# Kernel optimization log

Measured on AMD Instinct MI355X. Metric: run time of the kernel, lower is better.

Reference implementation:

```python
import jax, jax.numpy as jnp
import numpy as np

B, S, D, E, H, K = 64, 2048, 1024, 32, 4096, 8


def setup_inputs() -> dict:
    key = jax.random.key(0)
    k0, k1, k2, k3 = jax.random.split(key, 4)
    x = jax.random.normal(k0, (B, S, D), jnp.float32)
    # gate: nn.Linear(D, E) -> weight [E, D], bias [E]
    gate_w = jax.random.normal(k1, (E, D), jnp.float32) * (1.0 / np.sqrt(D))
    gate_b = jnp.zeros((E,), jnp.float32)
    # expert weights include the bias row (input dim + 1)
    w1 = jax.random.normal(k2, (E, D + 1, H), jnp.float32) * (1.0 / np.sqrt(D + 1))
    w2 = jax.random.normal(k3, (E, H + 1, D), jnp.float32) * (1.0 / np.sqrt(H + 1))
    return {"x": x, "gate_w": gate_w, "gate_b": gate_b, "w1": w1, "w2": w2}


def reference(x, gate_w, gate_b, w1, w2):
    b, s, d = x.shape
    # gating: softmax over the TOKEN axis (expert-choice routing)
    logits = jnp.einsum('bsd,ed->bse', x, gate_w) + gate_b          # [b, s, E]
    probs = jax.nn.softmax(logits, axis=-2)                          # softmax over tokens
    # top-k tokens per expert (torch.topk over dim=-2)
    vals_t, idx_t = jax.lax.top_k(probs.transpose(0, 2, 1), K)      # [b, E, k]
    vals = vals_t.transpose(0, 2, 1)                                 # [b, k, E]
    idx = idx_t.transpose(0, 2, 1)                                   # [b, k, E]
    flat_idx = idx.reshape(b, K * E)                                 # gather order: [k, E] flattened
    # gather selected tokens
    tok = jnp.take_along_axis(x, flat_idx[:, :, None], axis=1)       # [b, k*E, d]
    tok = tok.reshape(b, K, E, d)
    # weighted merge (mux) of the k tokens per expert
    merged = jnp.einsum('bked,bke->bed', tok, vals)                  # [b, E, d]
    ones = jnp.ones(merged.shape[:-1] + (1,), merged.dtype)
    # expert FFN (bias folded into the extra weight row)
    h = jnp.einsum('bei,eih->beh', jnp.concatenate([merged, ones], -1), w1)
    h = jax.nn.gelu(h, approximate=False)                            # torch nn.GELU() = exact erf
    o = jnp.einsum('bej,ejo->beo', jnp.concatenate([h, ones], -1), w2)  # [b, E, d]
    # demux: broadcast expert output back to its k tokens, weighted, scatter-add
    out_tok = jnp.einsum('beo,bke->bkeo', o, vals).reshape(b, K * E, d)
    out = jnp.zeros_like(x).at[jnp.arange(b)[:, None], flat_idx].add(out_tok)
    return out
```

## Files before the change

### kernel.cpp

```cpp
#include <hip/hip_runtime.h>
#include <hip/hip_bf16.h>
#include <math.h>

constexpr int NB = 64;
constexpr int NS = 2048;
constexpr int ND = 1024;
constexpr int NE = 32;
constexpr int NH = 4096;
constexpr int NK = 8;

typedef short bf16x8 __attribute__((ext_vector_type(8)));
typedef float f32x4  __attribute__((ext_vector_type(4)));

__device__ __forceinline__ unsigned short f2bf_rne(float v) {
  unsigned u = __builtin_bit_cast(unsigned, v);
  u += 0x7fffu + ((u >> 16) & 1u);
  return (unsigned short)(u >> 16);
}

__device__ __forceinline__ void gload_lds16(const void* g, void* l) {
  __builtin_amdgcn_global_load_lds(
      (const __attribute__((address_space(1))) unsigned*)g,
      (__attribute__((address_space(3))) unsigned*)l, 16, 0, 0);
}

__global__ __launch_bounds__(256) void k_gate_mfma(const float* __restrict__ x,
                                                   const float* __restrict__ gw,
                                                   float* __restrict__ logitsT) {
  const int b  = blockIdx.y;
  const int s0 = blockIdx.x * 128;
  const int t  = threadIdx.x;
  const int l  = t & 63;
  const int w  = t >> 6;

  __shared__ char smem[40960];
  float* trans = (float*)smem;

  f32x4 acc[2][2] = {};

  const int xr_ = t >> 4, xc = (t & 15) * 4;
  const int ge = t >> 3,  gk = (t & 7) * 8;

  float xA[8][4], xB[8][4], wA[8], wB[8];

  auto issue = [&](int kt, float (&xreg)[8][4], float (&wreg)[8]) {
    const int k0 = kt * 64;
#pragma unroll
    for (int p = 0; p < 8; ++p) {
      const int r = p * 16 + xr_;
      *(float4*)xreg[p] = *(const float4*)&x[((size_t)b * NS + s0 + r) * ND + k0 + xc];
    }
    *(float4*)&wreg[0] = *(const float4*)&gw[(size_t)ge * ND + k0 + gk];
    *(float4*)&wreg[4] = *(const float4*)&gw[(size_t)ge * ND + k0 + gk + 4];
  };
  auto commit = [&](int dst, float (&xreg)[8][4], float (&wreg)[8]) {
    short* Ah = (short*)(smem + dst * 16384);
    short* Bh = (short*)(smem + 32768 + dst * 4096);
#pragma unroll
    for (int p = 0; p < 8; ++p) {
      const int r = p * 16 + xr_;
      unsigned short h[4];
#pragma unroll
      for (int j = 0; j < 4; ++j) h[j] = f2bf_rne(xreg[p][j]);
      const int off = r * 64 + (xc ^ ((r & 7) * 8));
      *(ushort4*)&Ah[off] = *(const ushort4*)h;
    }
    unsigned short h8[8];
#pragma unroll
    for (int j = 0; j < 8; ++j) h8[j] = f2bf_rne(wreg[j]);
    const int boff = ge * 64 + (gk ^ ((ge & 7) * 8));
    *(uint4*)&Bh[boff] = *(const uint4*)h8;
  };
  auto mfma_phase = [&](int cur) {
    const short* Ah = (const short*)(smem + cur * 16384);
    const short* Bh = (const short*)(smem + 32768 + cur * 4096);
#pragma unroll
    for (int ks = 0; ks < 2; ++ks) {
      const int koff = ks * 32 + (l >> 4) * 8;
      bf16x8 a[2], bb[2];
#pragma unroll
      for (int mf = 0; mf < 2; ++mf) {
        const int r = w * 32 + mf * 16 + (l & 15);
        a[mf] = *(const bf16x8*)&Ah[r * 64 + (koff ^ ((r & 7) * 8))];
      }
#pragma unroll
      for (int nf = 0; nf < 2; ++nf) {
        const int n = nf * 16 + (l & 15);
        bb[nf] = *(const bf16x8*)&Bh[n * 64 + (koff ^ ((n & 7) * 8))];
      }
#pragma unroll
      for (int mf = 0; mf < 2; ++mf)
#pragma unroll
        for (int nf = 0; nf < 2; ++nf)
          acc[mf][nf] = __builtin_amdgcn_mfma_f32_16x16x32_bf16(a[mf], bb[nf], acc[mf][nf], 0, 0, 0);
    }
  };
  auto bar = [&]() {
    asm volatile("s_waitcnt lgkmcnt(0)" ::: "memory");
    __builtin_amdgcn_s_barrier();
    __builtin_amdgcn_sched_barrier(0);
  };

  issue(0, xA, wA);
  issue(1, xB, wB);
  commit(0, xA, wA);
  bar();

  for (int kt = 0; kt < ND / 64; kt += 2) {
    if (kt + 2 < ND / 64) issue(kt + 2, xA, wA);
    commit(1, xB, wB);
    mfma_phase(0);
    bar();
    if (kt + 3 < ND / 64) issue(kt + 3, xB, wB);
    if (kt + 2 < ND / 64) commit(0, xA, wA);
    mfma_phase(1);
    bar();
  }

#pragma unroll
  for (int mf = 0; mf < 2; ++mf)
#pragma unroll
    for (int nf = 0; nf < 2; ++nf)
#pragma unroll
      for (int j = 0; j < 4; ++j) {
        const int sl = w * 32 + mf * 16 + (l >> 4) * 4 + j;
        const int ec = nf * 16 + (l & 15);
        trans[sl * 33 + ec] = acc[mf][nf][j];
      }
  __syncthreads();
  const int eo = t >> 3, sc = (t & 7) * 16;
#pragma unroll
  for (int j4 = 0; j4 < 4; ++j4) {
    float4 v;
    v.x = trans[(sc + j4 * 4 + 0) * 33 + eo];
    v.y = trans[(sc + j4 * 4 + 1) * 33 + eo];
    v.z = trans[(sc + j4 * 4 + 2) * 33 + eo];
    v.w = trans[(sc + j4 * 4 + 3) * 33 + eo];
    *(float4*)&logitsT[((size_t)b * NE + eo) * NS + s0 + sc + j4 * 4] = v;
  }
}

__global__ __launch_bounds__(256) void k_topk(const float* __restrict__ logitsT,
                                              const float* __restrict__ x,
                                              const float* __restrict__ gw,
                                              float* __restrict__ tval,
                                              int* __restrict__ tidx) {
  const int be = blockIdx.x, b = be >> 5, e = be & 31;
  const float* row = logitsT + (size_t)be * NS;
  const int t = threadIdx.x, w = t >> 6, lane = t & 63;

  __shared__ float  cv[64];
  __shared__ int    cix[64];
  __shared__ double wsum[4];
  __shared__ float  smax;
  __shared__ int    gci[16];
  __shared__ float  glc[16];
  __shared__ double ginv;

  float v[8]; int si[8];
#pragma unroll
  for (int j = 0; j < 8; ++j) {
    const int s = w * 512 + lane + j * 64;
    v[j] = row[s]; si[j] = s;
  }
#pragma unroll
  for (int i = 0; i < 7; ++i)
#pragma unroll
    for (int j = 0; j < 7 - i; ++j) {
      const bool sw = (v[j + 1] > v[j]) || (v[j + 1] == v[j] && si[j + 1] < si[j]);
      const float tv = sw ? v[j + 1] : v[j];
      const int   ti = sw ? si[j + 1] : si[j];
      v[j + 1] = sw ? v[j] : v[j + 1];  si[j + 1] = sw ? si[j] : si[j + 1];
      v[j] = tv;  si[j] = ti;
    }
  const float mxl = v[0];
  double s8 = 1.0;
#pragma unroll
  for (int j = 1; j < 8; ++j) s8 += (double)expf(v[j] - mxl);

  for (int r = 0; r < 16; ++r) {
    float bp = v[0]; int bi = si[0]; int bl = lane;
#pragma unroll
    for (int off = 1; off < 64; off <<= 1) {
      const float op = __shfl_xor(bp, off);
      const int   oi = __shfl_xor(bi, off);
      const int   ol = __shfl_xor(bl, off);
      if (op > bp || (op == bp && oi < bi)) { bp = op; bi = oi; bl = ol; }
    }
    if (lane == 0) { cv[w * 16 + r] = bp; cix[w * 16 + r] = bi; }
    if (lane == bl) {
      v[0]=v[1]; v[1]=v[2]; v[2]=v[3]; v[3]=v[4]; v[4]=v[5]; v[5]=v[6]; v[6]=v[7]; v[7]=-INFINITY;
      si[0]=si[1]; si[1]=si[2]; si[2]=si[3]; si[3]=si[4]; si[4]=si[5]; si[5]=si[6]; si[6]=si[7]; si[7]=0x7fffffff;
    }
  }
  __syncthreads();
  if (w == 0) {
    float mv = cv[lane]; int mi = cix[lane];
    for (int r = 0; r < 16; ++r) {
      float bp = mv; int bi = mi; int bl = lane;
#pragma unroll
      for (int off = 1; off < 64; off <<= 1) {
        const float op = __shfl_xor(bp, off);
        const int   oi = __shfl_xor(bi, off);
        const int   ol = __shfl_xor(bl, off);
        if (op > bp || (op == bp && oi < bi)) { bp = op; bi = oi; bl = ol; }
      }
      if (lane == 0) { gci[r] = bi; if (r == 0) smax = bp; }
      if (lane == bl) { mv = -INFINITY; mi = 0x7fffffff; }
    }
  }
  __syncthreads();
  const float mx = smax;
  double lsum = s8 * (double)expf(mxl - mx);
#pragma unroll
  for (int off = 32; off; off >>= 1) lsum += __shfl_xor(lsum, off);
  if (lane == 0) wsum[w] = lsum;
  __syncthreads();
  if (t == 0) ginv = 1.0 / (wsum[0] + wsum[1] + wsum[2] + wsum[3]);

  const int kb = lane * 16;
  float gwl[16];
  *(float4*)&gwl[0]  = *(const float4*)&gw[(size_t)e * ND + kb];
  *(float4*)&gwl[4]  = *(const float4*)&gw[(size_t)e * ND + kb + 4];
  *(float4*)&gwl[8]  = *(const float4*)&gw[(size_t)e * ND + kb + 8];
  *(float4*)&gwl[12] = *(const float4*)&gw[(size_t)e * ND + kb + 12];
#pragma unroll
  for (int q = 0; q < 4; ++q) {
    const int c = w * 4 + q;
    const int ciq = gci[c];
    const float* xr = x + ((size_t)b * NS + ciq) * ND + kb;
    float xv[16];
    *(float4*)&xv[0]  = *(const float4*)&xr[0];
    *(float4*)&xv[4]  = *(const float4*)&xr[4];
    *(float4*)&xv[8]  = *(const float4*)&xr[8];
    *(float4*)&xv[12] = *(const float4*)&xr[12];
    double d = 0.0;
#pragma unroll
    for (int j2 = 0; j2 < 16; ++j2) d += (double)xv[j2] * (double)gwl[j2];
#pragma unroll
    for (int off = 32; off; off >>= 1) d += __shfl_xor(d, off);
    if (lane == 0) glc[c] = (float)d;
  }
  __syncthreads();
  if (t < 16) {
    const float mylc = glc[t]; const int myci = gci[t];
    int rank = 0;
#pragma unroll
    for (int c2 = 0; c2 < 16; ++c2) {
      if (c2 == t) continue;
      rank += (glc[c2] > mylc) || (glc[c2] == mylc && gci[c2] < myci);
    }
    if (rank < 8) {
      tval[be * 8 + rank] = (float)((double)expf(mylc - mx) * ginv);
      tidx[be * 8 + rank] = myci;
    }
  }
}

__global__ __launch_bounds__(256) void k_merge(const float* __restrict__ x,
                                               const float* __restrict__ tval,
                                               const int* __restrict__ tidx,
                                               unsigned short* __restrict__ A1) {
  const int be = blockIdx.x;
  const int b  = be >> 5;
  const int e  = be & 31;
  const int t  = threadIdx.x;
  float4 acc = {0.f, 0.f, 0.f, 0.f};
#pragma unroll
  for (int k = 0; k < 8; ++k) {
    float v = tval[be * 8 + k];
    int   s = tidx[be * 8 + k];
    float4 xv = *(const float4*)&x[((size_t)b * NS + s) * ND + t * 4];
    acc.x += v * xv.x; acc.y += v * xv.y; acc.z += v * xv.z; acc.w += v * xv.w;
  }
  const int kt = t >> 4;
  const int g  = (t & 15) >> 1;
  const size_t off = ((size_t)(e * 16 + kt)) * 4096 + b * 64 + ((g ^ (b & 7)) << 3) + (t & 1) * 4;
  unsigned short h4[4] = {f2bf_rne(acc.x), f2bf_rne(acc.y), f2bf_rne(acc.z), f2bf_rne(acc.w)};
  *(ushort4*)&A1[off] = *(const ushort4*)h4;
}

template <int K, int N, bool GELU>
__global__ __launch_bounds__(256, 4) void k_ffn(const unsigned short* __restrict__ AT,
                                                const float* __restrict__ W,
                                                unsigned short* __restrict__ OT,
                                                float* __restrict__ Of) {
  constexpr int KT = K / 64;
  const int e  = blockIdx.y;
  const int n0 = blockIdx.x * 64;
  const int t  = threadIdx.x, l = t & 63, w = t >> 6;
  const int wr = w >> 1, wc = w & 1;

  __shared__ char smem[32768];

  const float* Wbase = W + (size_t)e * (K + 1) * N;
  f32x4 acc[2][2] = {};

  const int wn  = l;
  const int wk0 = w * 8;
  float wreg[2][8];

  auto issueW = [&](int kt) {
    const float* Wg = Wbase + (size_t)(kt * 64) * N + n0 + wn;
#pragma unroll
    for (int rn = 0; rn < 2; ++rn)
#pragma unroll
      for (int j = 0; j < 8; ++j)
        wreg[rn][j] = Wg[(size_t)(wk0 + rn * 32 + j) * N];
  };
  auto issueA = [&](int kt, int dst) {
    const unsigned short* at = AT + ((size_t)(e * KT + kt)) * 4096;
    char* Ab = smem + dst * 8192;
#pragma unroll
    for (int p = 0; p < 2; ++p)
      gload_lds16(at + p * 2048 + t * 8, Ab + p * 4096 + w * 1024);
  };
  auto commitW = [&](int dst) {
    short* Bb = (short*)(smem + 16384 + dst * 8192);
#pragma unroll
    for (int rn = 0; rn < 2; ++rn) {
      const int kr = (wk0 + rn * 32) >> 3;
      unsigned short s8[8];
#pragma unroll
      for (int j = 0; j < 8; ++j) s8[j] = f2bf_rne(wreg[rn][j]);
      *(uint4*)&Bb[wn * 64 + ((kr ^ (wn & 7)) << 3)] = *(const uint4*)s8;
    }
  };
  auto mfma_phase = [&](int cur) {
    const short* Ab = (const short*)(smem + cur * 8192);
    const short* Bb = (const short*)(smem + 16384 + cur * 8192);
#pragma unroll
    for (int ks = 0; ks < 2; ++ks) {
      const int g8 = ks * 4 + (l >> 4);
      bf16x8 a[2], bb[2];
#pragma unroll
      for (int mf = 0; mf < 2; ++mf) {
        const int m = wr * 32 + mf * 16 + (l & 15);
        a[mf] = *(const bf16x8*)&Ab[m * 64 + ((g8 ^ (m & 7)) << 3)];
      }
#pragma unroll
      for (int nf = 0; nf < 2; ++nf) {
        const int n = wc * 32 + nf * 16 + (l & 15);
        bb[nf] = *(const bf16x8*)&Bb[n * 64 + ((g8 ^ (n & 7)) << 3)];
      }
#pragma unroll
      for (int mf = 0; mf < 2; ++mf)
#pragma unroll
        for (int nf = 0; nf < 2; ++nf)
          acc[mf][nf] = __builtin_amdgcn_mfma_f32_16x16x32_bf16(a[mf], bb[nf], acc[mf][nf], 0, 0, 0);
    }
  };

  issueW(0); issueA(0, 0);
  commitW(0);
  __syncthreads();
  int cur = 0;
  for (int kt = 0; kt < KT; ++kt) {
    const bool more = (kt + 1 < KT);
    if (more) { issueW(kt + 1); issueA(kt + 1, cur ^ 1); }
    mfma_phase(cur);
    if (more) commitW(cur ^ 1);
    __syncthreads();
    cur ^= 1;
  }

  if (GELU) {
    unsigned short* transU = (unsigned short*)smem;
#pragma unroll
    for (int nf = 0; nf < 2; ++nf) {
      const int c = wc * 32 + nf * 16 + (l & 15);
      const float bias = Wbase[(size_t)K * N + n0 + c];
#pragma unroll
      for (int mf = 0; mf < 2; ++mf)
#pragma unroll
        for (int j = 0; j < 4; ++j) {
          const int m = wr * 32 + mf * 16 + (l >> 4) * 4 + j;
          float vv = acc[mf][nf][j] + bias;
          vv = 0.5f * vv * (1.0f + erff(vv * 0.70710678118654752440f));
          transU[m * 72 + c] = f2bf_rne(vv);
        }
    }
    __syncthreads();
    const int m  = t >> 2;
    const int c0 = (t & 3) * 16;
    const size_t tb = ((size_t)(e * (N / 64) + blockIdx.x)) * 4096;
    uint4 v0 = *(const uint4*)&transU[m * 72 + c0];
    uint4 v1 = *(const uint4*)&transU[m * 72 + c0 + 8];
    const int g0 = c0 >> 3;
    *(uint4*)&OT[tb + m * 64 + ((g0 ^ (m & 7)) << 3)]       = v0;
    *(uint4*)&OT[tb + m * 64 + (((g0 + 1) ^ (m & 7)) << 3)] = v1;
  } else {
    float* transF = (float*)smem;
#pragma unroll
    for (int nf = 0; nf < 2; ++nf) {
      const int c = wc * 32 + nf * 16 + (l & 15);
      const float bias = Wbase[(size_t)K * N + n0 + c];
#pragma unroll
      for (int mf = 0; mf < 2; ++mf)
#pragma unroll
        for (int j = 0; j < 4; ++j) {
          const int m = wr * 32 + mf * 16 + (l >> 4) * 4 + j;
          transF[m * 68 + c] = acc[mf][nf][j] + bias;
        }
    }
    __syncthreads();
    const int m  = t >> 2;
    const int c0 = (t & 3) * 16;
    float* og = Of + ((size_t)m * NE + e) * ND + n0 + c0;
    *(float4*)&og[0]  = *(const float4*)&transF[m * 68 + c0];
    *(float4*)&og[4]  = *(const float4*)&transF[m * 68 + c0 + 4];
    *(float4*)&og[8]  = *(const float4*)&transF[m * 68 + c0 + 8];
    *(float4*)&og[12] = *(const float4*)&transF[m * 68 + c0 + 12];
  }
}

__global__ __launch_bounds__(256) void k_scatter(const float* __restrict__ Obuf,
                                                 const float* __restrict__ tval,
                                                 const int* __restrict__ tidx,
                                                 float* __restrict__ out) {
  const int s0 = blockIdx.x * 8;
  const int b  = blockIdx.y;
  const int t  = threadIdx.x;
  const int w  = t >> 6;
  __shared__ unsigned long long masks[8][4];

  const int myIdx = tidx[b * 256 + t];
#pragma unroll
  for (int j = 0; j < 8; ++j) {
    unsigned long long m = __ballot(myIdx == s0 + j);
    if ((t & 63) == 0) masks[j][w] = m;
  }
  __syncthreads();

#pragma unroll
  for (int j = 0; j < 8; ++j) {
    float4 acc = {0.f, 0.f, 0.f, 0.f};
#pragma unroll
    for (int q = 0; q < 4; ++q) {
      unsigned long long mm = masks[j][q];
      while (mm) {
        int bit = __ffsll(mm) - 1;
        mm &= mm - 1;
        int r = q * 64 + bit;
        float v = tval[b * 256 + r];
        const float4 ov = *(const float4*)&Obuf[((size_t)b * NE + (r >> 3)) * ND + t * 4];
        acc.x += v * ov.x; acc.y += v * ov.y; acc.z += v * ov.z; acc.w += v * ov.w;
      }
    }
    *(float4*)&out[((size_t)b * NS + s0 + j) * ND + t * 4] = acc;
  }
}

extern "C" void kernel_launch(void* const* d_in, const int* in_sizes, int n_in,
                              void* d_out, int out_size, void* d_ws, size_t ws_size,
                              hipStream_t stream) {
  const float* x  = (const float*)d_in[0];
  const float* gw = (const float*)d_in[1];
  const float* w1 = (const float*)d_in[3];
  const float* w2 = (const float*)d_in[4];
  float* out = (float*)d_out;

  char* ws = (char*)d_ws;
  float* logitsT     = (float*)ws;
  float* tval        = (float*)(ws + 16777216);
  int*   tidx        = (int*)  (ws + 16842752);
  unsigned short* A1 = (unsigned short*)(ws + 16908288);
  unsigned short* Hb = (unsigned short*)(ws + 21102592);
  float* Obuf        = (float*)(ws + 37879808);

  k_gate_mfma<<<dim3(NS / 128, NB), 256, 0, stream>>>(x, gw, logitsT);
  k_topk<<<NB * NE, 256, 0, stream>>>(logitsT, x, gw, tval, tidx);
  k_merge<<<NB * NE, 256, 0, stream>>>(x, tval, tidx, A1);
  k_ffn<ND, NH, true ><<<dim3(NH / 64, NE), 256, 0, stream>>>(A1, w1, Hb, nullptr);
  k_ffn<NH, ND, false><<<dim3(ND / 64, NE), 256, 0, stream>>>(Hb, w2, nullptr, Obuf);
  k_scatter<<<dim3(NS / 8, NB), 256, 0, stream>>>(Obuf, tval, tidx, out);
}
```

Measured before the change: 545.8 us.

## Halve gate GEMM tile height and pack top-k keys into 64-bit shuffles

The gate logits kernel now processes 64 tokens per block instead of 128, which doubles the grid and halves LDS use and register staging. This is meant to raise occupancy and memory-level parallelism on the x read, at the cost of reloading the gate weights more often. The top-k kernel encodes value and index into one order-preserving 64-bit key, so each shuffle reduction step moves one word instead of three. The final 64-candidate merge becomes a rank count per lane rather than 16 serial wave reductions.

After: 514.1 us. 5.8% less time.

```diff
diff --git a/kernel.cpp b/kernel.cpp
--- a/kernel.cpp
+++ b/kernel.cpp
@@ -24,75 +24,74 @@
       (__attribute__((address_space(3))) unsigned*)l, 16, 0, 0);
 }
 
+__device__ __forceinline__ unsigned ford(float f) {
+  unsigned u = __builtin_bit_cast(unsigned, f);
+  return (u & 0x80000000u) ? ~u : (u | 0x80000000u);
+}
+__device__ __forceinline__ float finv(unsigned o) {
+  unsigned u = (o & 0x80000000u) ? (o & 0x7fffffffu) : ~o;
+  return __builtin_bit_cast(float, u);
+}
+
 __global__ __launch_bounds__(256) void k_gate_mfma(const float* __restrict__ x,
                                                    const float* __restrict__ gw,
                                                    float* __restrict__ logitsT) {
   const int b  = blockIdx.y;
-  const int s0 = blockIdx.x * 128;
+  const int s0 = blockIdx.x * 64;
   const int t  = threadIdx.x;
   const int l  = t & 63;
   const int w  = t >> 6;
 
-  __shared__ char smem[40960];
+  __shared__ char smem[24576];
   float* trans = (float*)smem;
 
-  f32x4 acc[2][2] = {};
-
-  const int xr_ = t >> 4, xc = (t & 15) * 4;
-  const int ge = t >> 3,  gk = (t & 7) * 8;
-
-  float xA[8][4], xB[8][4], wA[8], wB[8];
-
-  auto issue = [&](int kt, float (&xreg)[8][4], float (&wreg)[8]) {
+  f32x4 acc[2] = {};
+
+  const int ar  = t >> 2;
+  const int ac4 = (t & 3) * 16;
+  const int ge  = t >> 3;
+  const int gk  = (t & 7) * 8;
+
+  float xA[4][4], xB[4][4], wA[8], wB[8];
+
+  auto issue = [&](int kt, float (&xreg)[4][4], float (&wreg)[8]) {
     const int k0 = kt * 64;
-#pragma unroll
-    for (int p = 0; p < 8; ++p) {
-      const int r = p * 16 + xr_;
-      *(float4*)xreg[p] = *(const float4*)&x[((size_t)b * NS + s0 + r) * ND + k0 + xc];
-    }
+    const float* xr = &x[((size_t)b * NS + s0 + ar) * ND + k0 + ac4];
+#pragma unroll
+    for (int j = 0; j < 4; ++j) *(float4*)xreg[j] = *(const float4*)&xr[j * 4];
     *(float4*)&wreg[0] = *(const float4*)&gw[(size_t)ge * ND + k0 + gk];
     *(float4*)&wreg[4] = *(const float4*)&gw[(size_t)ge * ND + k0 + gk + 4];
   };
-  auto commit = [&](int dst, float (&xreg)[8][4], float (&wreg)[8]) {
-    short* Ah = (short*)(smem + dst * 16384);
-    short* Bh = (short*)(smem + 32768 + dst * 4096);
-#pragma unroll
-    for (int p = 0; p < 8; ++p) {
-      const int r = p * 16 + xr_;
+  auto commit = [&](int dst, float (&xreg)[4][4], float (&wreg)[8]) {
+    short* Ah = (short*)(smem + dst * 8192);
+    short* Bh = (short*)(smem + 16384 + dst * 4096);
+#pragma unroll
+    for (int j = 0; j < 4; ++j) {
       unsigned short h[4];
 #pragma unroll
-      for (int j = 0; j < 4; ++j) h[j] = f2bf_rne(xreg[p][j]);
-      const int off = r * 64 + (xc ^ ((r & 7) * 8));
-      *(ushort4*)&Ah[off] = *(const ushort4*)h;
+      for (int q = 0; q < 4; ++q) h[q] = f2bf_rne(xreg[j][q]);
+      const int col = ac4 + j * 4;
+      *(ushort4*)&Ah[ar * 64 + (col ^ ((ar & 7) * 8))] = *(const ushort4*)h;
     }
     unsigned short h8[8];
 #pragma unroll
     for (int j = 0; j < 8; ++j) h8[j] = f2bf_rne(wreg[j]);
-    const int boff = ge * 64 + (gk ^ ((ge & 7) * 8));
-    *(uint4*)&Bh[boff] = *(const uint4*)h8;
+    *(uint4*)&Bh[ge * 64 + (gk ^ ((ge & 7) * 8))] = *(const uint4*)h8;
   };
   auto mfma_phase = [&](int cur) {
-    const short* Ah = (const short*)(smem + cur * 16384);
-    const short* Bh = (const short*)(smem + 32768 + cur * 4096);
+    const short* Ah = (const short*)(smem + cur * 8192);
+    const short* Bh = (const short*)(smem + 16384 + cur * 4096);
 #pragma unroll
     for (int ks = 0; ks < 2; ++ks) {
       const int koff = ks * 32 + (l >> 4) * 8;
-      bf16x8 a[2], bb[2];
-#pragma unroll
-      for (int mf = 0; mf < 2; ++mf) {
-        const int r = w * 32 + mf * 16 + (l & 15);
-        a[mf] = *(const bf16x8*)&Ah[r * 64 + (koff ^ ((r & 7) * 8))];
-      }
+      const int rl = w * 16 + (l & 15);
+      bf16x8 a = *(const bf16x8*)&Ah[rl * 64 + (koff ^ ((rl & 7) * 8))];
 #pragma unroll
       for (int nf = 0; nf < 2; ++nf) {
         const int n = nf * 16 + (l & 15);
-        bb[nf] = *(const bf16x8*)&Bh[n * 64 + (koff ^ ((n & 7) * 8))];
+        bf16x8 bb = *(const bf16x8*)&Bh[n * 64 + (koff ^ ((n & 7) * 8))];
+        acc[nf] = __builtin_amdgcn_mfma_f32_16x16x32_bf16(a, bb, acc[nf], 0, 0, 0);
       }
-#pragma unroll
-      for (int mf = 0; mf < 2; ++mf)
-#pragma unroll
-        for (int nf = 0; nf < 2; ++nf)
-          acc[mf][nf] = __builtin_amdgcn_mfma_f32_16x16x32_bf16(a[mf], bb[nf], acc[mf][nf], 0, 0, 0);
     }
   };
   auto bar = [&]() {
@@ -118,25 +117,23 @@
   }
 
 #pragma unroll
-  for (int mf = 0; mf < 2; ++mf)
-#pragma unroll
-    for (int nf = 0; nf < 2; ++nf)
-#pragma unroll
-      for (int j = 0; j < 4; ++j) {
-        const int sl = w * 32 + mf * 16 + (l >> 4) * 4 + j;
-        const int ec = nf * 16 + (l & 15);
-        trans[sl * 33 + ec] = acc[mf][nf][j];
-      }
-  __syncthreads();
-  const int eo = t >> 3, sc = (t & 7) * 16;
-#pragma unroll
-  for (int j4 = 0; j4 < 4; ++j4) {
+  for (int nf = 0; nf < 2; ++nf)
+#pragma unroll
+    for (int j = 0; j < 4; ++j) {
+      const int sl = w * 16 + (l >> 4) * 4 + j;
+      const int ec = nf * 16 + (l & 15);
+      trans[sl * 33 + ec] = acc[nf][j];
+    }
+  __syncthreads();
+  const int eo = t >> 3, sc = (t & 7) * 8;
+#pragma unroll
+  for (int q = 0; q < 2; ++q) {
     float4 v;
-    v.x = trans[(sc + j4 * 4 + 0) * 33 + eo];
-    v.y = trans[(sc + j4 * 4 + 1) * 33 + eo];
-    v.z = trans[(sc + j4 * 4 + 2) * 33 + eo];
-    v.w = trans[(sc + j4 * 4 + 3) * 33 + eo];
-    *(float4*)&logitsT[((size_t)b * NE + eo) * NS + s0 + sc + j4 * 4] = v;
+    v.x = trans[(sc + q * 4 + 0) * 33 + eo];
+    v.y = trans[(sc + q * 4 + 1) * 33 + eo];
+    v.z = trans[(sc + q * 4 + 2) * 33 + eo];
+    v.w = trans[(sc + q * 4 + 3) * 33 + eo];
+    *(float4*)&logitsT[((size_t)b * NE + eo) * NS + s0 + sc + q * 4] = v;
   }
 }
 
@@ -149,12 +146,12 @@
   const float* row = logitsT + (size_t)be * NS;
   const int t = threadIdx.x, w = t >> 6, lane = t & 63;
 
-  __shared__ float  cv[64];
-  __shared__ int    cix[64];
-  __shared__ double wsum[4];
-  __shared__ float  smax;
+  __shared__ unsigned long long cvp[64];
+  __shared__ unsigned long long gcp[16];
   __shared__ int    gci[16];
   __shared__ float  glc[16];
+  __shared__ double wsum[4];
+  __shared__ float  smax_s;
   __shared__ double ginv;
 
   float v[8]; int si[8];
@@ -178,39 +175,39 @@
 #pragma unroll
   for (int j = 1; j < 8; ++j) s8 += (double)expf(v[j] - mxl);
 
+  unsigned long long p[8];
+#pragma unroll
+  for (int j = 0; j < 8; ++j)
+    p[j] = ((unsigned long long)ford(v[j]) << 32) | (0xFFFFFFFFu - (unsigned)si[j]);
+
   for (int r = 0; r < 16; ++r) {
-    float bp = v[0]; int bi = si[0]; int bl = lane;
+    unsigned long long m = p[0];
 #pragma unroll
     for (int off = 1; off < 64; off <<= 1) {
-      const float op = __shfl_xor(bp, off);
-      const int   oi = __shfl_xor(bi, off);
-      const int   ol = __shfl_xor(bl, off);
-      if (op > bp || (op == bp && oi < bi)) { bp = op; bi = oi; bl = ol; }
-    }
-    if (lane == 0) { cv[w * 16 + r] = bp; cix[w * 16 + r] = bi; }
-    if (lane == bl) {
-      v[0]=v[1]; v[1]=v[2]; v[2]=v[3]; v[3]=v[4]; v[4]=v[5]; v[5]=v[6]; v[6]=v[7]; v[7]=-INFINITY;
-      si[0]=si[1]; si[1]=si[2]; si[2]=si[3]; si[3]=si[4]; si[4]=si[5]; si[5]=si[6]; si[6]=si[7]; si[7]=0x7fffffff;
-    }
-  }
-  __syncthreads();
+      const unsigned long long o = __shfl_xor(m, off);
+      m = (o > m) ? o : m;
+    }
+    if (lane == 0) cvp[w * 16 + r] = m;
+    if (p[0] == m) {
+      p[0]=p[1]; p[1]=p[2]; p[2]=p[3]; p[3]=p[4]; p[4]=p[5]; p[5]=p[6]; p[6]=p[7]; p[7]=0ull;
+    }
+  }
+  __syncthreads();
+
   if (w == 0) {
-    float mv = cv[lane]; int mi = cix[lane];
-    for (int r = 0; r < 16; ++r) {
-      float bp = mv; int bi = mi; int bl = lane;
-#pragma unroll
-      for (int off = 1; off < 64; off <<= 1) {
-        const float op = __shfl_xor(bp, off);
-        const int   oi = __shfl_xor(bi, off);
-        const int   ol = __shfl_xor(bl, off);
-        if (op > bp || (op == bp && oi < bi)) { bp = op; bi = oi; bl = ol; }
-      }
-      if (lane == 0) { gci[r] = bi; if (r == 0) smax = bp; }
-      if (lane == bl) { mv = -INFINITY; mi = 0x7fffffff; }
-    }
-  }
-  __syncthreads();
-  const float mx = smax;
+    const unsigned long long mine = cvp[lane];
+    int rank = 0;
+#pragma unroll
+    for (int j = 0; j < 64; ++j) rank += (cvp[j] > mine);
+    if (rank < 16) {
+      gcp[rank] = mine;
+      gci[rank] = (int)(0xFFFFFFFFu - (unsigned)(mine & 0xFFFFFFFFu));
+      if (rank == 0) smax_s = finv((unsigned)(mine >> 32));
+    }
+  }
+  __syncthreads();
+
+  const float mx = smax_s;
   double lsum = s8 * (double)expf(mxl - mx);
 #pragma unroll
   for (int off = 32; off; off >>= 1) lsum += __shfl_xor(lsum, off);
@@ -468,7 +465,7 @@
   unsigned short* Hb = (unsigned short*)(ws + 21102592);
   float* Obuf        = (float*)(ws + 37879808);
 
-  k_gate_mfma<<<dim3(NS / 128, NB), 256, 0, stream>>>(x, gw, logitsT);
+  k_gate_mfma<<<dim3(NS / 64, NB), 256, 0, stream>>>(x, gw, logitsT);
   k_topk<<<NB * NE, 256, 0, stream>>>(logitsT, x, gw, tval, tidx);
   k_merge<<<NB * NE, 256, 0, stream>>>(x, tval, tidx, A1);
   k_ffn<ND, NH, true ><<<dim3(NH / 64, NE), 256, 0, stream>>>(A1, w1, Hb, nullptr);
```
